# Optimization experiments

Hardware: AMD Instinct MI355X
Metric: run time of the kernel (lower is better)

The kernel has to match this reference:

```python
import jax, jax.numpy as jnp
import numpy as np

WEIGHT = 0.2
EPS_MAG = 1e-8   # sqrt eps in magnitude
EPS_NORM = 1e-12 # F.normalize default eps
EPS_COS = 1e-8   # F.cosine_similarity default eps


def _sobel_kernels(C, dtype):
    smooth = np.array([1.0, 2.0, 1.0], np.float32)
    deriv = np.array([-1.0, 0.0, 1.0], np.float32)
    kx = np.einsum('d,h,w->dhw', smooth, smooth, deriv)
    ky = np.einsum('d,h,w->dhw', smooth, deriv, smooth)
    kz = np.einsum('d,h,w->dhw', deriv, smooth, smooth)
    # depthwise kernels: OIDHW with O=C, I=1 (feature_group_count=C)
    return [jnp.asarray(np.broadcast_to(k[None, None], (C, 1, 3, 3, 3)).copy(), dtype)
            for k in (kx, ky, kz)]


def _grads(x, kernels):
    C = x.shape[1]
    dn = jax.lax.conv_dimension_numbers(x.shape, kernels[0].shape,
                                        ('NCDHW', 'OIDHW', 'NCDHW'))
    return [jax.lax.conv_general_dilated(x, k, window_strides=(1, 1, 1),
                                         padding=[(1, 1)] * 3,
                                         dimension_numbers=dn,
                                         feature_group_count=C)
            for k in kernels]


def setup_inputs() -> dict:
    key = jax.random.key(0)
    k1, k2 = jax.random.split(key)
    shape = (2, 1, 160, 160, 160)
    return {
        'pred': jax.random.normal(k1, shape, dtype=jnp.float32),
        'target': jax.random.normal(k2, shape, dtype=jnp.float32),
    }


def reference(pred, target):
    C = pred.shape[1]
    kernels = _sobel_kernels(C, pred.dtype)
    pg = jnp.stack(_grads(pred, kernels), axis=1)    # (B, 3, C, D, H, W)
    tg = jnp.stack(_grads(target, kernels), axis=1)  # (B, 3, C, D, H, W)

    pred_mag = jnp.sqrt(jnp.sum(pg * pg, axis=1) + EPS_MAG)
    targ_mag = jnp.sqrt(jnp.sum(tg * tg, axis=1) + EPS_MAG)
    magnitude_loss = jnp.mean((pred_mag - targ_mag) ** 2)

    # F.normalize(p=2, dim=1): x / max(||x||, eps)
    pn = pg / jnp.maximum(jnp.linalg.norm(pg, axis=1, keepdims=True), EPS_NORM)
    tn = tg / jnp.maximum(jnp.linalg.norm(tg, axis=1, keepdims=True), EPS_NORM)

    # F.cosine_similarity(dim=1): dot / (max(||a||,eps) * max(||b||,eps))
    dot = jnp.sum(pn * tn, axis=1)
    na = jnp.maximum(jnp.linalg.norm(pn, axis=1), EPS_COS)
    nb = jnp.maximum(jnp.linalg.norm(tn, axis=1), EPS_COS)
    direction_loss = 1.0 - jnp.mean(dot / (na * nb))

    return WEIGHT * (magnitude_loss + direction_loss)
```

## Files before the change

kernel.cpp:

```cpp
#include <hip/hip_runtime.h>


constexpr int Dd = 160, Hh = 160, Ww = 160;
constexpr int TW = 32, TH = 16, DC = 16;
constexpr int NTX = Ww / TW;
constexpr int NTY = Hh / TH;
constexpr int NTZ = Dd / DC;
constexpr int NBLOCKS = NTX * NTY * NTZ * 2;
constexpr int NXCD = 8;
constexpr int CHUNK = NBLOCKS / NXCD;
constexpr int PLANES = DC + 2;
constexpr int PLSZ = Hh * Ww;
constexpr double NVOX = 2.0 * Dd * Hh * Ww;

constexpr int SPANF = 40;
constexpr int SROWS = TH + 2;
constexpr int VOLF  = 768;

typedef float v2 __attribute__((ext_vector_type(2)));
typedef float v4 __attribute__((ext_vector_type(4)));

#define GLD16(g, l)                                                     \
    __builtin_amdgcn_global_load_lds(                                   \
        (const __attribute__((address_space(1))) void*)(g),             \
        (__attribute__((address_space(3))) void*)(l), 16, 0, 0)

__global__ __launch_bounds__(256)
void acl_partial(const float* __restrict__ pred, const float* __restrict__ targ,
                 float2* __restrict__ partial)
{
    __shared__ float sv[2][2][VOLF];
    __shared__ float rred[8];

    const int tid  = threadIdx.x;
    const int lane = tid & 63;
    const int wid  = tid >> 6;
    const int gx   = tid & 15;
    const int r    = tid >> 4;

    const int bid = blockIdx.x;
    const int swz = (bid % NXCD) * CHUNK + bid / NXCD;
    const int zt  = swz % NTZ;
    const int t1  = swz / NTZ;
    const int wt  = t1 % NTX;
    const int t2  = t1 / NTX;
    const int ht  = t2 % NTY;
    const int b   = t2 / NTY;

    const int x0 = wt * TW, y0 = ht * TH;
    const int z0 = zt * DC;
    const size_t base = (size_t)b * ((size_t)Dd * PLSZ);
    const float* __restrict__ pv = pred + base;
    const float* __restrict__ tv = targ + base;

    const int so   = (wid < 3 ? wid : 0) * 1024 + lane * 16;
    int srow = so / 160;  if (srow > SROWS - 1) srow = SROWS - 1;
    const int scol = (so % 160) >> 2;
    int sgy = y0 - 1 + srow;  sgy = sgy < 0 ? 0 : (sgy > Hh - 1 ? Hh - 1 : sgy);
    int sgx = x0 - 4 + scol;  sgx = sgx < 0 ? 0 : (sgx > Ww - 4 ? Ww - 4 : sgx);
    const int splaneoff = sgy * Ww + sgx;
    const int ldsoff = wid * 256;

    const bool blkLo = (x0 == 0);
    const bool blkHi = (x0 + TW == Ww);
    const bool fixLo = blkLo && (gx == 0);
    const bool fixHi = blkHi && (gx == 15);
    const bool yokm  = (y0 + r - 1 >= 0);
    const bool yokp  = (y0 + r + 1 < Hh);
    const int  rb    = r * SPANF + 2 * gx + 3;

    const v2 z2 = {0.f, 0.f};
    const v4 z4 = {0.f, 0.f, 0.f, 0.f};

    v2 P1x = z2, P1y = z2, P1z = z2, P2x = z2, P2y = z2, P2z = z2;
    v2 T1x = z2, T1y = z2, T1z = z2, T2x = z2, T2y = z2, T2z = z2;
    v2 accm = z2, accc = z2;

    auto stage = [&](int p1, int buf) {
        if (wid < 3) {
            int gz = z0 - 1 + p1;
            gz = gz < 0 ? 0 : (gz > Dd - 1 ? Dd - 1 : gz);
            const float* gp = pv + (ptrdiff_t)gz * PLSZ + splaneoff;
            const float* gt = tv + (ptrdiff_t)gz * PLSZ + splaneoff;
            GLD16(gp, &sv[buf][0][ldsoff]);
            GLD16(gt, &sv[buf][1][ldsoff]);
        }
    };

    auto loadRow = [&](const float* S, int idx, bool valid) -> v4 {
        v4 row;
        row.x = fixLo ? 0.f : S[idx];
        row.y = S[idx + 1];
        row.z = S[idx + 2];
        row.w = fixHi ? 0.f : S[idx + 3];
        if (!valid) row = z4;
        return row;
    };

    auto consumeVol = [&](const float* S, v2& A, v2& B, v2& C) {
        const v4 m = loadRow(S, rb,             yokm);
        const v4 c = loadRow(S, rb + SPANF,     true);
        const v4 p = loadRow(S, rb + 2 * SPANF, yokp);
        const v2 HSm = m.xy + 2.f*m.yz + m.zw;
        const v2 HDm = m.zw - m.xy;
        const v2 HS0 = c.xy + 2.f*c.yz + c.zw;
        const v2 HD0 = c.zw - c.xy;
        const v2 HSp = p.xy + 2.f*p.yz + p.zw;
        const v2 HDp = p.zw - p.xy;
        A = HSm + 2.f*HS0 + HSp;
        B = HDm + 2.f*HD0 + HDp;
        C = HSp - HSm;
    };

    stage(0, 0);
    __syncthreads();

    #pragma unroll 1
    for (int p = 0; p < PLANES; ++p) {
        const int buf = p & 1;

        if (p + 1 < PLANES) stage(p + 1, buf ^ 1);

        const bool zok = ((unsigned)(z0 - 1 + p) < (unsigned)Dd);

        v2 A, B, C;
        consumeVol(&sv[buf][0][0], A, B, C);
        if (!zok) { A = z2; B = z2; C = z2; }
        const v2 fpx = P1x + B, fpy = P1y + C, fpz = A - P1z;
        P1x = 2.f*B + P2x;  P1y = 2.f*C + P2y;  P1z = P2z;
        P2x = B;  P2y = C;  P2z = A;

        consumeVol(&sv[buf][1][0], A, B, C);
        if (!zok) { A = z2; B = z2; C = z2; }
        const v2 ftx = T1x + B, fty = T1y + C, ftz = A - T1z;
        T1x = 2.f*B + T2x;  T1y = 2.f*C + T2y;  T1z = T2z;
        T2x = B;  T2y = C;  T2z = A;

        if (p >= 2) {
            const v2 np2 = fpx*fpx + fpy*fpy + fpz*fpz;
            const v2 nt2 = ftx*ftx + fty*fty + ftz*ftz;
            const v2 a  = np2 + 1e-8f;
            const v2 bb = nt2 + 1e-8f;
            const v2 ab = a * bb;
            v2 rt;
            rt.x = __builtin_amdgcn_sqrtf(ab.x);
            rt.y = __builtin_amdgcn_sqrtf(ab.y);
            accm += a + bb - 2.f*rt;
            const v2 dt = fpx*ftx + fpy*fty + fpz*ftz;
            v2 pr = np2 * nt2;
            pr.x = fmaxf(pr.x, 1e-30f);
            pr.y = fmaxf(pr.y, 1e-30f);
            v2 rq;
            rq.x = __builtin_amdgcn_rsqf(pr.x);
            rq.y = __builtin_amdgcn_rsqf(pr.y);
            accc += dt * rq;
        }

        __syncthreads();
    }

    float am = accm.x + accm.y;
    float ac = accc.x + accc.y;
    #pragma unroll
    for (int off = 32; off >= 1; off >>= 1) {
        am += __shfl_down(am, off);
        ac += __shfl_down(ac, off);
    }
    if ((tid & 63) == 0) { rred[wid] = am; rred[4 + wid] = ac; }
    __syncthreads();
    if (tid == 0) {
        const float m = rred[0] + rred[1] + rred[2] + rred[3];
        const float c = rred[4] + rred[5] + rred[6] + rred[7];
        partial[bid] = make_float2(m, c);
    }
}

__global__ __launch_bounds__(256)
void acl_final(const float2* __restrict__ partial, float* __restrict__ out)
{
    __shared__ double sm[256], sc[256];
    double m = 0.0, c = 0.0;
    for (int i = threadIdx.x; i < NBLOCKS; i += 256) {
        const float2 v = partial[i];
        m += (double)v.x;
        c += (double)v.y;
    }
    sm[threadIdx.x] = m;
    sc[threadIdx.x] = c;
    __syncthreads();
    #pragma unroll
    for (int s = 128; s >= 1; s >>= 1) {
        if (threadIdx.x < (unsigned)s) {
            sm[threadIdx.x] += sm[threadIdx.x + s];
            sc[threadIdx.x] += sc[threadIdx.x + s];
        }
        __syncthreads();
    }
    if (threadIdx.x == 0) {
        const double mag_loss = sm[0] / NVOX;
        const double dir_loss = 1.0 - sc[0] / NVOX;
        out[0] = (float)(0.2 * (mag_loss + dir_loss));
    }
}

extern "C" void kernel_launch(void* const* d_in, const int* in_sizes, int n_in,
                              void* d_out, int out_size, void* d_ws, size_t ws_size,
                              hipStream_t stream) {
    const float* pred = (const float*)d_in[0];
    const float* targ = (const float*)d_in[1];
    float* out = (float*)d_out;
    float2* partial = (float2*)d_ws;

    acl_partial<<<NBLOCKS, 256, 0, stream>>>(pred, targ, partial);
    acl_final<<<1, 256, 0, stream>>>(partial, out);
}
```

Baseline: 32.55 us.

## Give each wave a private LDS halo slab and drop block-wide barriers

Each of the four waves now stages its own 6-row by 40-float slab of pred and target per plane into private LDS, covering its 4 output rows plus y-halo. Cross-wave __syncthreads in the plane loop are replaced by a per-wave s_waitcnt vmcnt(0). The goal is to let waves run independently without barrier stalls. In exchange, halo rows are loaded redundantly across waves (24 staged rows instead of 18), and the wait on outstanding loads happens before the next prefetch is issued, which limits overlap of load and compute.

```diff
diff --git a/kernel.cpp b/kernel.cpp
--- a/kernel.cpp
+++ b/kernel.cpp
@@ -14,8 +14,9 @@
 constexpr double NVOX = 2.0 * Dd * Hh * Ww;
 
 constexpr int SPANF = 40;
-constexpr int SROWS = TH + 2;
-constexpr int VOLF  = 768;
+constexpr int WROWS = 6;
+constexpr int WVOLD = WROWS * SPANF;
+constexpr int WVOLF = 256;
 
 typedef float v2 __attribute__((ext_vector_type(2)));
 typedef float v4 __attribute__((ext_vector_type(4)));
@@ -29,14 +30,14 @@
 void acl_partial(const float* __restrict__ pred, const float* __restrict__ targ,
                  float2* __restrict__ partial)
 {
-    __shared__ float sv[2][2][VOLF];
+    __shared__ float sv[4][2][2][WVOLF];
     __shared__ float rred[8];
 
     const int tid  = threadIdx.x;
     const int lane = tid & 63;
-    const int wid  = tid >> 6;
-    const int gx   = tid & 15;
-    const int r    = tid >> 4;
+    const int w    = tid >> 6;
+    const int gx   = lane & 15;
+    const int lw   = lane >> 4;
 
     const int bid = blockIdx.x;
     const int swz = (bid % NXCD) * CHUNK + bid / NXCD;
@@ -53,21 +54,22 @@
     const float* __restrict__ pv = pred + base;
     const float* __restrict__ tv = targ + base;
 
-    const int so   = (wid < 3 ? wid : 0) * 1024 + lane * 16;
-    int srow = so / 160;  if (srow > SROWS - 1) srow = SROWS - 1;
-    const int scol = (so % 160) >> 2;
-    int sgy = y0 - 1 + srow;  sgy = sgy < 0 ? 0 : (sgy > Hh - 1 ? Hh - 1 : sgy);
-    int sgx = x0 - 4 + scol;  sgx = sgx < 0 ? 0 : (sgx > Ww - 4 ? Ww - 4 : sgx);
+    const int wr0 = y0 + 4 * w - 1;
+    int d = lane * 4;  if (d > WVOLD - 4) d = WVOLD - 4;
+    const int srow = d / SPANF;
+    const int scol = d - srow * SPANF;
+    int sgy = wr0 + srow;  sgy = sgy < 0 ? 0 : (sgy > Hh - 1 ? Hh - 1 : sgy);
+    int sgx = x0 - 4 + scol; sgx = sgx < 0 ? 0 : (sgx > Ww - 4 ? Ww - 4 : sgx);
     const int splaneoff = sgy * Ww + sgx;
-    const int ldsoff = wid * 256;
 
     const bool blkLo = (x0 == 0);
     const bool blkHi = (x0 + TW == Ww);
     const bool fixLo = blkLo && (gx == 0);
     const bool fixHi = blkHi && (gx == 15);
-    const bool yokm  = (y0 + r - 1 >= 0);
-    const bool yokp  = (y0 + r + 1 < Hh);
-    const int  rb    = r * SPANF + 2 * gx + 3;
+    const int  gr    = y0 + 4 * w + lw;
+    const bool yokm  = (gr - 1 >= 0);
+    const bool yokp  = (gr + 1 < Hh);
+    const int  rb    = lw * SPANF + 2 * gx + 3;
 
     const v2 z2 = {0.f, 0.f};
     const v4 z4 = {0.f, 0.f, 0.f, 0.f};
@@ -77,14 +79,10 @@
     v2 accm = z2, accc = z2;
 
     auto stage = [&](int p1, int buf) {
-        if (wid < 3) {
-            int gz = z0 - 1 + p1;
-            gz = gz < 0 ? 0 : (gz > Dd - 1 ? Dd - 1 : gz);
-            const float* gp = pv + (ptrdiff_t)gz * PLSZ + splaneoff;
-            const float* gt = tv + (ptrdiff_t)gz * PLSZ + splaneoff;
-            GLD16(gp, &sv[buf][0][ldsoff]);
-            GLD16(gt, &sv[buf][1][ldsoff]);
-        }
+        int gz = z0 - 1 + p1;
+        gz = gz < 0 ? 0 : (gz > Dd - 1 ? Dd - 1 : gz);
+        GLD16(pv + (ptrdiff_t)gz * PLSZ + splaneoff, &sv[w][buf][0][0]);
+        GLD16(tv + (ptrdiff_t)gz * PLSZ + splaneoff, &sv[w][buf][1][0]);
     };
 
     auto loadRow = [&](const float* S, int idx, bool valid) -> v4 {
@@ -113,24 +111,26 @@
     };
 
     stage(0, 0);
-    __syncthreads();
 
     #pragma unroll 1
     for (int p = 0; p < PLANES; ++p) {
         const int buf = p & 1;
 
+        asm volatile("s_waitcnt vmcnt(0)" ::: "memory");
+        __builtin_amdgcn_sched_barrier(0);
+
         if (p + 1 < PLANES) stage(p + 1, buf ^ 1);
 
         const bool zok = ((unsigned)(z0 - 1 + p) < (unsigned)Dd);
 
         v2 A, B, C;
-        consumeVol(&sv[buf][0][0], A, B, C);
+        consumeVol(&sv[w][buf][0][0], A, B, C);
         if (!zok) { A = z2; B = z2; C = z2; }
         const v2 fpx = P1x + B, fpy = P1y + C, fpz = A - P1z;
         P1x = 2.f*B + P2x;  P1y = 2.f*C + P2y;  P1z = P2z;
         P2x = B;  P2y = C;  P2z = A;
 
-        consumeVol(&sv[buf][1][0], A, B, C);
+        consumeVol(&sv[w][buf][1][0], A, B, C);
         if (!zok) { A = z2; B = z2; C = z2; }
         const v2 ftx = T1x + B, fty = T1y + C, ftz = A - T1z;
         T1x = 2.f*B + T2x;  T1y = 2.f*C + T2y;  T1z = T2z;
@@ -155,8 +155,6 @@
             rq.y = __builtin_amdgcn_rsqf(pr.y);
             accc += dt * rq;
         }
-
-        __syncthreads();
     }
 
     float am = accm.x + accm.y;
@@ -166,7 +164,7 @@
         am += __shfl_down(am, off);
         ac += __shfl_down(ac, off);
     }
-    if ((tid & 63) == 0) { rred[wid] = am; rred[4 + wid] = ac; }
+    if ((tid & 63) == 0) { rred[w] = am; rred[4 + w] = ac; }
     __syncthreads();
     if (tid == 0) {
         const float m = rred[0] + rred[1] + rred[2] + rred[3];
```

Measured after the change: 31.74 us. 2.5% less time.

## Precompute horizontal Sobel combos per row into LDS with register-prefetched loads

Applied to the files above, without the earlier changes.

Replaces the direct global-to-LDS staging of raw planes with register loads (issued two planes ahead) by 144 threads. Each of these threads computes the horizontal smooth and difference terms for its row segment and writes them to LDS as padded float4 entries. Consumers then read three vec4 combos per field, instead of assembling 4-wide rows with scalar LDS reads, which avoids redundant horizontal work and cuts LDS read traffic. In exchange, the global loads are unaligned vector loads held in registers across the loop, and some threads sit idle during the combo phase.

```diff
diff --git a/kernel.cpp b/kernel.cpp
--- a/kernel.cpp
+++ b/kernel.cpp
@@ -13,30 +13,25 @@
 constexpr int PLSZ = Hh * Ww;
 constexpr double NVOX = 2.0 * Dd * Hh * Ww;
 
-constexpr int SPANF = 40;
-constexpr int SROWS = TH + 2;
-constexpr int VOLF  = 768;
+constexpr int CROWS = TH + 2;
+constexpr int CGP   = 17;
+constexpr int NITEM = CROWS * 8;
 
 typedef float v2 __attribute__((ext_vector_type(2)));
 typedef float v4 __attribute__((ext_vector_type(4)));
-
-#define GLD16(g, l)                                                     \
-    __builtin_amdgcn_global_load_lds(                                   \
-        (const __attribute__((address_space(1))) void*)(g),             \
-        (__attribute__((address_space(3))) void*)(l), 16, 0, 0)
+typedef float v4a __attribute__((ext_vector_type(4), aligned(4)));
+typedef float v2a __attribute__((ext_vector_type(2), aligned(4)));
 
 __global__ __launch_bounds__(256)
 void acl_partial(const float* __restrict__ pred, const float* __restrict__ targ,
                  float2* __restrict__ partial)
 {
-    __shared__ float sv[2][2][VOLF];
+    __shared__ v4 cmb[2][2][CROWS][CGP];
     __shared__ float rred[8];
 
-    const int tid  = threadIdx.x;
-    const int lane = tid & 63;
-    const int wid  = tid >> 6;
-    const int gx   = tid & 15;
-    const int r    = tid >> 4;
+    const int tid = threadIdx.x;
+    const int gx  = tid & 15;
+    const int r   = tid >> 4;
 
     const int bid = blockIdx.x;
     const int swz = (bid % NXCD) * CHUNK + bid / NXCD;
@@ -53,21 +48,17 @@
     const float* __restrict__ pv = pred + base;
     const float* __restrict__ tv = targ + base;
 
-    const int so   = (wid < 3 ? wid : 0) * 1024 + lane * 16;
-    int srow = so / 160;  if (srow > SROWS - 1) srow = SROWS - 1;
-    const int scol = (so % 160) >> 2;
-    int sgy = y0 - 1 + srow;  sgy = sgy < 0 ? 0 : (sgy > Hh - 1 ? Hh - 1 : sgy);
-    int sgx = x0 - 4 + scol;  sgx = sgx < 0 ? 0 : (sgx > Ww - 4 ? Ww - 4 : sgx);
-    const int splaneoff = sgy * Ww + sgx;
-    const int ldsoff = wid * 256;
-
-    const bool blkLo = (x0 == 0);
-    const bool blkHi = (x0 + TW == Ww);
-    const bool fixLo = blkLo && (gx == 0);
-    const bool fixHi = blkHi && (gx == 15);
-    const bool yokm  = (y0 + r - 1 >= 0);
-    const bool yokp  = (y0 + r + 1 < Hh);
-    const int  rb    = r * SPANF + 2 * gx + 3;
+    const bool hasItem = (tid < NITEM);
+    const int crow = tid >> 3;
+    const int cg   = tid & 7;
+    const int gyc  = y0 - 1 + crow;
+    const bool yokc = hasItem && (gyc >= 0) && (gyc < Hh);
+    int gycl = gyc < 0 ? 0 : (gyc > Hh - 1 ? Hh - 1 : gyc);
+    const bool fixLo = (x0 == 0) && (cg == 0);
+    const bool fixHi = (x0 + TW == Ww) && (cg == 7);
+    const int xb = x0 + 4 * cg - 1;
+    const int a4 = gycl * Ww + (fixLo ? 0 : xb);
+    const int a2 = gycl * Ww + (fixHi ? (Ww - 2) : (xb + 4));
 
     const v2 z2 = {0.f, 0.f};
     const v4 z4 = {0.f, 0.f, 0.f, 0.f};
@@ -76,85 +67,101 @@
     v2 T1x = z2, T1y = z2, T1z = z2, T2x = z2, T2y = z2, T2z = z2;
     v2 accm = z2, accc = z2;
 
-    auto stage = [&](int p1, int buf) {
-        if (wid < 3) {
-            int gz = z0 - 1 + p1;
+    v4 pr4 = z4, tr4 = z4;
+    v2 pr2 = z2, tr2 = z2;
+
+    auto issueG = [&](int p2) {
+        if (hasItem) {
+            int gz = z0 - 1 + p2;
             gz = gz < 0 ? 0 : (gz > Dd - 1 ? Dd - 1 : gz);
-            const float* gp = pv + (ptrdiff_t)gz * PLSZ + splaneoff;
-            const float* gt = tv + (ptrdiff_t)gz * PLSZ + splaneoff;
-            GLD16(gp, &sv[buf][0][ldsoff]);
-            GLD16(gt, &sv[buf][1][ldsoff]);
-        }
-    };
-
-    auto loadRow = [&](const float* S, int idx, bool valid) -> v4 {
-        v4 row;
-        row.x = fixLo ? 0.f : S[idx];
-        row.y = S[idx + 1];
-        row.z = S[idx + 2];
-        row.w = fixHi ? 0.f : S[idx + 3];
-        if (!valid) row = z4;
-        return row;
-    };
-
-    auto consumeVol = [&](const float* S, v2& A, v2& B, v2& C) {
-        const v4 m = loadRow(S, rb,             yokm);
-        const v4 c = loadRow(S, rb + SPANF,     true);
-        const v4 p = loadRow(S, rb + 2 * SPANF, yokp);
-        const v2 HSm = m.xy + 2.f*m.yz + m.zw;
-        const v2 HDm = m.zw - m.xy;
-        const v2 HS0 = c.xy + 2.f*c.yz + c.zw;
-        const v2 HD0 = c.zw - c.xy;
-        const v2 HSp = p.xy + 2.f*p.yz + p.zw;
-        const v2 HDp = p.zw - p.xy;
-        A = HSm + 2.f*HS0 + HSp;
-        B = HDm + 2.f*HD0 + HDp;
-        C = HSp - HSm;
-    };
-
-    stage(0, 0);
+            const float* pz = pv + (ptrdiff_t)gz * PLSZ;
+            const float* tz = tv + (ptrdiff_t)gz * PLSZ;
+            pr4 = *(const v4a*)(pz + a4);  pr2 = *(const v2a*)(pz + a2);
+            tr4 = *(const v4a*)(tz + a4);  tr2 = *(const v2a*)(tz + a2);
+        }
+    };
+
+    auto comboOne = [&](const v4 v, const v2 u, v4& w0, v4& w1) {
+        float e0, e1, e2, e3, e4, e5;
+        if (fixLo)      { e0 = 0.f;  e1 = v.x; e2 = v.y; e3 = v.z; e4 = v.w; e5 = u.y; }
+        else if (fixHi) { e0 = v.x;  e1 = v.y; e2 = v.z; e3 = v.w; e4 = u.y; e5 = 0.f; }
+        else            { e0 = v.x;  e1 = v.y; e2 = v.z; e3 = v.w; e4 = u.x; e5 = u.y; }
+        const float HS0 = e0 + 2.f*e1 + e2, HS1 = e1 + 2.f*e2 + e3;
+        const float HS2 = e2 + 2.f*e3 + e4, HS3 = e3 + 2.f*e4 + e5;
+        w0 = (v4){HS0, HS1, e2 - e0, e3 - e1};
+        w1 = (v4){HS2, HS3, e4 - e2, e5 - e3};
+    };
+
+    auto comboWrite = [&](int p1, int slot) {
+        const bool zokc = ((unsigned)(z0 - 1 + p1) < (unsigned)Dd);
+        const bool valid = zokc && yokc;
+        v4 w0, w1;
+        comboOne(pr4, pr2, w0, w1);
+        if (!valid) { w0 = z4; w1 = z4; }
+        if (hasItem) {
+            cmb[slot][0][crow][2 * cg]     = w0;
+            cmb[slot][0][crow][2 * cg + 1] = w1;
+        }
+        comboOne(tr4, tr2, w0, w1);
+        if (!valid) { w0 = z4; w1 = z4; }
+        if (hasItem) {
+            cmb[slot][1][crow][2 * cg]     = w0;
+            cmb[slot][1][crow][2 * cg + 1] = w1;
+        }
+    };
+
+    auto consume = [&](int p, int s) {
+        {
+            const v4 qm = cmb[s][0][r][gx], q0 = cmb[s][0][r + 1][gx], qp = cmb[s][0][r + 2][gx];
+            const v2 A = qm.xy + 2.f*q0.xy + qp.xy;
+            const v2 B = qm.zw + 2.f*q0.zw + qp.zw;
+            const v2 C = qp.xy - qm.xy;
+            const v2 fpx = P1x + B, fpy = P1y + C, fpz = A - P1z;
+            P1x = 2.f*B + P2x;  P1y = 2.f*C + P2y;  P1z = P2z;
+            P2x = B;  P2y = C;  P2z = A;
+            const v4 sm_ = cmb[s][1][r][gx], s0_ = cmb[s][1][r + 1][gx], sp_ = cmb[s][1][r + 2][gx];
+            const v2 At = sm_.xy + 2.f*s0_.xy + sp_.xy;
+            const v2 Bt = sm_.zw + 2.f*s0_.zw + sp_.zw;
+            const v2 Ct = sp_.xy - sm_.xy;
+            const v2 ftx = T1x + Bt, fty = T1y + Ct, ftz = At - T1z;
+            T1x = 2.f*Bt + T2x;  T1y = 2.f*Ct + T2y;  T1z = T2z;
+            T2x = Bt;  T2y = Ct;  T2z = At;
+
+            if (p >= 2) {
+                const v2 np2 = fpx*fpx + fpy*fpy + fpz*fpz;
+                const v2 nt2 = ftx*ftx + fty*fty + ftz*ftz;
+                const v2 a  = np2 + 1e-8f;
+                const v2 bb = nt2 + 1e-8f;
+                const v2 ab = a * bb;
+                v2 rt;
+                rt.x = __builtin_amdgcn_sqrtf(ab.x);
+                rt.y = __builtin_amdgcn_sqrtf(ab.y);
+                accm += a + bb - 2.f*rt;
+                const v2 dt = fpx*ftx + fpy*fty + fpz*ftz;
+                v2 pr = np2 * nt2;
+                pr.x = fmaxf(pr.x, 1e-30f);
+                pr.y = fmaxf(pr.y, 1e-30f);
+                v2 rq;
+                rq.x = __builtin_amdgcn_rsqf(pr.x);
+                rq.y = __builtin_amdgcn_rsqf(pr.y);
+                accc += dt * rq;
+            }
+        }
+    };
+
+    issueG(0);
+    comboWrite(0, 0);
+    issueG(1);
     __syncthreads();
 
     #pragma unroll 1
     for (int p = 0; p < PLANES; ++p) {
-        const int buf = p & 1;
-
-        if (p + 1 < PLANES) stage(p + 1, buf ^ 1);
-
-        const bool zok = ((unsigned)(z0 - 1 + p) < (unsigned)Dd);
-
-        v2 A, B, C;
-        consumeVol(&sv[buf][0][0], A, B, C);
-        if (!zok) { A = z2; B = z2; C = z2; }
-        const v2 fpx = P1x + B, fpy = P1y + C, fpz = A - P1z;
-        P1x = 2.f*B + P2x;  P1y = 2.f*C + P2y;  P1z = P2z;
-        P2x = B;  P2y = C;  P2z = A;
-
-        consumeVol(&sv[buf][1][0], A, B, C);
-        if (!zok) { A = z2; B = z2; C = z2; }
-        const v2 ftx = T1x + B, fty = T1y + C, ftz = A - T1z;
-        T1x = 2.f*B + T2x;  T1y = 2.f*C + T2y;  T1z = T2z;
-        T2x = B;  T2y = C;  T2z = A;
-
-        if (p >= 2) {
-            const v2 np2 = fpx*fpx + fpy*fpy + fpz*fpz;
-            const v2 nt2 = ftx*ftx + fty*fty + ftz*ftz;
-            const v2 a  = np2 + 1e-8f;
-            const v2 bb = nt2 + 1e-8f;
-            const v2 ab = a * bb;
-            v2 rt;
-            rt.x = __builtin_amdgcn_sqrtf(ab.x);
-            rt.y = __builtin_amdgcn_sqrtf(ab.y);
-            accm += a + bb - 2.f*rt;
-            const v2 dt = fpx*ftx + fpy*fty + fpz*ftz;
-            v2 pr = np2 * nt2;
-            pr.x = fmaxf(pr.x, 1e-30f);
-            pr.y = fmaxf(pr.y, 1e-30f);
-            v2 rq;
-            rq.x = __builtin_amdgcn_rsqf(pr.x);
-            rq.y = __builtin_amdgcn_rsqf(pr.y);
-            accc += dt * rq;
-        }
+        const int s = p & 1;
+
+        consume(p, s);
+
+        if (p + 1 < PLANES) comboWrite(p + 1, s ^ 1);
+        if (p + 2 < PLANES) issueG(p + 2);
 
         __syncthreads();
     }
@@ -166,6 +173,7 @@
         am += __shfl_down(am, off);
         ac += __shfl_down(ac, off);
     }
+    const int wid = tid >> 6;
     if ((tid & 63) == 0) { rred[wid] = am; rred[4 + wid] = ac; }
     __syncthreads();
     if (tid == 0) {
```

Result: faster. 29.45 us (-9.5%).
